# Optimization experiments

Hardware: AMD Instinct MI355X
Metric: run time of the kernel (lower is better)

## Reference

```python
import jax, jax.numpy as jnp
import numpy as np

B, C_IN, C_MID, C_OUT, H, W = 16, 128, 128, 128, 128, 128
DN = ('NCHW', 'OIHW', 'NCHW')


def conv1x1(x, w, b):
    y = jax.lax.conv_general_dilated(x, w, (1, 1), 'VALID', dimension_numbers=DN)
    return y + b[None, :, None, None]


def dwconv3(x, w, b):
    # depthwise 3x3, padding=1, groups = channels
    y = jax.lax.conv_general_dilated(x, w, (1, 1), ((1, 1), (1, 1)),
                                     feature_group_count=x.shape[1],
                                     dimension_numbers=DN)
    return y + b[None, :, None, None]


def setup_inputs() -> dict:
    key = jax.random.key(0)
    ks = jax.random.split(key, 15)
    s = 0.05
    return {
        'x':   jax.random.normal(ks[0], (B, C_IN, H, W), jnp.float32),
        'qw':  jax.random.normal(ks[1], (C_MID, C_IN, 1, 1), jnp.float32) * s,
        'qb':  jax.random.normal(ks[2], (C_MID,), jnp.float32) * s,
        'qdw': jax.random.normal(ks[3], (C_MID, 1, 3, 3), jnp.float32) * s,
        'qdb': jax.random.normal(ks[4], (C_MID,), jnp.float32) * s,
        'kw':  jax.random.normal(ks[5], (C_MID, C_IN, 1, 1), jnp.float32) * s,
        'kb':  jax.random.normal(ks[6], (C_MID,), jnp.float32) * s,
        'kdw': jax.random.normal(ks[7], (C_MID, 1, 3, 3), jnp.float32) * s,
        'kdb': jax.random.normal(ks[8], (C_MID,), jnp.float32) * s,
        'vw':  jax.random.normal(ks[9], (C_MID, C_IN, 1, 1), jnp.float32) * s,
        'vb':  jax.random.normal(ks[10], (C_MID,), jnp.float32) * s,
        'vdw': jax.random.normal(ks[11], (C_MID, 1, 3, 3), jnp.float32) * s,
        'vdb': jax.random.normal(ks[12], (C_MID,), jnp.float32) * s,
        'aw':  jax.random.normal(ks[13], (C_OUT, C_MID, 1, 1), jnp.float32) * s,
        'ab':  jax.random.normal(ks[14], (C_OUT,), jnp.float32) * s,
    }


def reference(x, qw, qb, qdw, qdb, kw, kb, kdw, kdb, vw, vb, vdw, vdb, aw, ab):
    b, c, h, w = x.shape
    q = dwconv3(conv1x1(x, qw, qb), qdw, qdb)
    k = dwconv3(conv1x1(x, kw, kb), kdw, kdb)
    v = dwconv3(conv1x1(x, vw, vb), vdw, vdb)
    # b c h w -> b c (h w)
    q = q.reshape(b, -1, h * w)
    k = k.reshape(b, -1, h * w)
    v = v.reshape(b, -1, h * w)
    # L2-normalize over spatial dim (torch F.normalize: x / max(||x||, eps))
    eps = 1e-12
    q = q / jnp.maximum(jnp.linalg.norm(q, axis=-1, keepdims=True), eps)
    k = k / jnp.maximum(jnp.linalg.norm(k, axis=-1, keepdims=True), eps)
    # channel-wise attention: [b, c, c]
    a = jax.nn.softmax(jnp.einsum('bcn,bdn->bcd', q, k), axis=-1)
    out = jnp.einsum('bcd,bdn->bcn', a, v).reshape(b, -1, h, w)
    return conv1x1(out, aw, ab)
```

## Files before the change

kernel.cpp:

```cpp
#include <hip/hip_runtime.h>

typedef unsigned short u16;
typedef unsigned int u32;
typedef __attribute__((ext_vector_type(8))) __bf16 bf16x8;
typedef __attribute__((ext_vector_type(4))) float f32x4;
typedef __attribute__((ext_vector_type(4))) u32 u32x4;
typedef __attribute__((ext_vector_type(2))) u32 u32x2;

#define HW 16384
#define C 128
#define NB 16
#define LSTR 136
#define FSTR 132

__device__ __forceinline__ u16 f2bf(float f) {
    __bf16 h = (__bf16)f;
    union { __bf16 h; u16 u; } c; c.h = h; return c.u;
}
__device__ __forceinline__ float bf2f(u16 u) {
    union { u32 i; float f; } c; c.i = ((u32)u) << 16; return c.f;
}

__device__ __forceinline__ bf16x8 load_wrow(const float* p) {
    f32x4 a = *(const f32x4*)p, b = *(const f32x4*)(p + 4);
    bf16x8 r;
    #pragma unroll
    for (int i = 0; i < 4; ++i) { r[i] = (__bf16)a[i]; r[i + 4] = (__bf16)b[i]; }
    return r;
}
__device__ __forceinline__ bf16x8 load_wrow(const u16* p) {
    return *(const bf16x8*)p;
}

template <typename WT, typename YT>
__device__ __forceinline__ void gemm128(
    const WT* __restrict__ W, const float* __restrict__ X,
    const float* __restrict__ bias, YT* __restrict__ Y,
    int n0, u16* lds)
{
    const int tid  = threadIdx.x;
    const int lane = tid & 63;
    const int wave = tid >> 6;
    const int m_lo = lane & 15;
    const int quad = lane >> 4;

    #pragma unroll
    for (int r = 0; r < 2; ++r) {
        int idx = tid + 256 * r;
        int n4  = idx & 31;
        int kc  = idx >> 5;
        const float* src = X + (size_t)(kc * 8) * HW + n0 + n4 * 4;
        f32x4 v[8];
        #pragma unroll
        for (int j = 0; j < 8; ++j) v[j] = *(const f32x4*)(src + (size_t)j * HW);
        #pragma unroll
        for (int t = 0; t < 4; ++t) {
            union { u16 u[8]; u32x4 q; } e;
            #pragma unroll
            for (int j = 0; j < 8; ++j) e.u[j] = f2bf(v[j][t]);
            int row = n4 * 4 + t;
            int cs  = kc ^ (n4 & 7);
            *(u32x4*)(lds + row * LSTR + cs * 8) = e.q;
        }
    }
    __syncthreads();

    f32x4 acc[2][8];
    #pragma unroll
    for (int mt = 0; mt < 2; ++mt)
        #pragma unroll
        for (int nt = 0; nt < 8; ++nt) {
            f32x4 z = {0.f, 0.f, 0.f, 0.f};
            acc[mt][nt] = z;
        }

    #pragma unroll
    for (int ks = 0; ks < 4; ++ks) {
        const int k0 = ks * 32 + quad * 8;
        bf16x8 af[2];
        #pragma unroll
        for (int mt = 0; mt < 2; ++mt) {
            int m = wave * 32 + mt * 16 + m_lo;
            af[mt] = load_wrow(W + (size_t)m * 128 + k0);
        }
        #pragma unroll
        for (int nt = 0; nt < 8; ++nt) {
            int n  = nt * 16 + m_lo;
            int cs = (ks * 4 + quad) ^ ((n >> 2) & 7);
            bf16x8 bfrag = *(const bf16x8*)(lds + n * LSTR + cs * 8);
            #pragma unroll
            for (int mt = 0; mt < 2; ++mt)
                acc[mt][nt] = __builtin_amdgcn_mfma_f32_16x16x32_bf16(
                    af[mt], bfrag, acc[mt][nt], 0, 0, 0);
        }
    }
    __syncthreads();

    if constexpr (sizeof(YT) == 2) {
        #pragma unroll
        for (int mt = 0; mt < 2; ++mt)
            #pragma unroll
            for (int nt = 0; nt < 8; ++nt)
                #pragma unroll
                for (int r = 0; r < 4; ++r) {
                    int m = wave * 32 + mt * 16 + quad * 4 + r;
                    int n = nt * 16 + m_lo;
                    lds[m * LSTR + n] = f2bf(acc[mt][nt][r] + bias[m]);
                }
        __syncthreads();
        #pragma unroll
        for (int i = 0; i < 8; ++i) {
            int idx = tid + 256 * i;
            int row = idx >> 4;
            int ch  = idx & 15;
            u32x4 v = *(u32x4*)(lds + row * LSTR + ch * 8);
            *(u32x4*)(Y + (size_t)row * HW + n0 + ch * 8) = v;
        }
    } else {
        float* ldsf = (float*)lds;
        #pragma unroll
        for (int ph = 0; ph < 2; ++ph) {
            if ((wave >> 1) == ph) {
                #pragma unroll
                for (int mt = 0; mt < 2; ++mt)
                    #pragma unroll
                    for (int nt = 0; nt < 8; ++nt)
                        #pragma unroll
                        for (int r = 0; r < 4; ++r) {
                            int m = wave * 32 + mt * 16 + quad * 4 + r;
                            int n = nt * 16 + m_lo;
                            ldsf[(m & 63) * FSTR + n] = acc[mt][nt][r] + bias[m];
                        }
            }
            __syncthreads();
            #pragma unroll
            for (int i = 0; i < 8; ++i) {
                int idx = tid + 256 * i;
                int row = idx >> 5;
                int c4  = idx & 31;
                f32x4 vv = *(const f32x4*)(ldsf + row * FSTR + c4 * 4);
                *(f32x4*)(Y + (size_t)(ph * 64 + row) * HW + n0 + c4 * 4) = vv;
            }
            __syncthreads();
        }
    }
}

__global__ __launch_bounds__(256) void k_conv_qk(
    const float* __restrict__ x,
    const float* __restrict__ qw, const float* __restrict__ qbias,
    const float* __restrict__ kw, const float* __restrict__ kbias,
    u16* __restrict__ qpl, u16* __restrict__ kpl)
{
    __shared__ __align__(16) u16 lds[128 * LSTR];
    int b = blockIdx.z, s = blockIdx.y;
    const float* W    = s ? kw : qw;
    const float* bias = s ? kbias : qbias;
    u16* Y = (s ? kpl : qpl) + (size_t)b * C * HW;
    gemm128(W, x + (size_t)b * C * HW, bias, Y, blockIdx.x * 128, lds);
}

__global__ __launch_bounds__(256) void k_conv_v(
    float* __restrict__ x, const float* __restrict__ vw, const float* __restrict__ vbias)
{
    __shared__ __align__(16) u16 lds[128 * LSTR];
    int b = blockIdx.z;
    float* Xb = x + (size_t)b * C * HW;
    gemm128(vw, Xb, vbias, Xb, blockIdx.x * 128, lds);
}

__global__ __launch_bounds__(256) void k_dw_qk(
    u16* __restrict__ qpl, u16* __restrict__ kpl,
    const float* __restrict__ qdw, const float* __restrict__ qdb,
    const float* __restrict__ kdw, const float* __restrict__ kdb,
    float* __restrict__ norm2)
{
    __shared__ __align__(16) u16 pl[HW];
    __shared__ float red[256];
    int pid = blockIdx.x;
    int s = pid >> 11, bc = pid & 2047, c = bc & 127;
    u16* plane = (s ? kpl : qpl) + (size_t)bc * HW;
    const float* dw = (s ? kdw : qdw) + c * 9;
    float bias = (s ? kdb : qdb)[c];
    int tid = threadIdx.x;

    #pragma unroll
    for (int i = 0; i < 8; ++i) {
        int idx = tid + 256 * i;
        *(u32x4*)(pl + idx * 8) = *(const u32x4*)(plane + idx * 8);
    }
    float w[9];
    #pragma unroll
    for (int j = 0; j < 9; ++j) w[j] = dw[j];
    __syncthreads();

    float ssq = 0.f;
    for (int i = 0; i < 16; ++i) {
        int p0 = (tid + 256 * i) * 4;
        int py = p0 >> 7, px0 = p0 & 127;
        float nb[3][6];
        #pragma unroll
        for (int dy = 0; dy < 3; ++dy) {
            int yy = py + dy - 1;
            bool yok = (yy >= 0) && (yy < 128);
            int ya = yok ? yy : 0;
            #pragma unroll
            for (int j = 0; j < 6; ++j) {
                int xx = px0 + j - 1;
                bool ok = yok && (xx >= 0) && (xx < 128);
                int xa = (xx >= 0 && xx < 128) ? xx : 0;
                float vv = bf2f(pl[ya * 128 + xa]);
                nb[dy][j] = ok ? vv : 0.f;
            }
        }
        u16 o[4];
        #pragma unroll
        for (int t = 0; t < 4; ++t) {
            float acc = bias;
            #pragma unroll
            for (int dy = 0; dy < 3; ++dy)
                #pragma unroll
                for (int dx = 0; dx < 3; ++dx)
                    acc += w[dy * 3 + dx] * nb[dy][t + dx];
            ssq += acc * acc;
            o[t] = f2bf(acc);
        }
        u32x2 pr;
        pr.x = (u32)o[0] | ((u32)o[1] << 16);
        pr.y = (u32)o[2] | ((u32)o[3] << 16);
        *(u32x2*)(plane + p0) = pr;
    }
    red[tid] = ssq;
    __syncthreads();
    for (int off = 128; off > 0; off >>= 1) {
        if (tid < off) red[tid] += red[tid + off];
        __syncthreads();
    }
    if (tid == 0) norm2[s * (NB * C) + bc] = red[0];
}

__global__ __launch_bounds__(256) void k_dw_v(
    float* __restrict__ x, const float* __restrict__ vdw, const float* __restrict__ vdb)
{
    __shared__ __align__(16) float pl[HW];
    int bc = blockIdx.x;
    int c = bc & 127;
    float* plane = x + (size_t)bc * HW;
    const float* dw = vdw + c * 9;
    float bias = vdb[c];
    int tid = threadIdx.x;

    #pragma unroll
    for (int i = 0; i < 16; ++i) {
        int idx = tid + 256 * i;
        *(f32x4*)(pl + idx * 4) = *(const f32x4*)(plane + idx * 4);
    }
    float w[9];
    #pragma unroll
    for (int j = 0; j < 9; ++j) w[j] = dw[j];
    __syncthreads();

    for (int i = 0; i < 16; ++i) {
        int p0 = (tid + 256 * i) * 4;
        int py = p0 >> 7, px0 = p0 & 127;
        float nb[3][6];
        #pragma unroll
        for (int dy = 0; dy < 3; ++dy) {
            int yy = py + dy - 1;
            bool yok = (yy >= 0) && (yy < 128);
            int ya = yok ? yy : 0;
            #pragma unroll
            for (int j = 0; j < 6; ++j) {
                int xx = px0 + j - 1;
                bool ok = yok && (xx >= 0) && (xx < 128);
                int xa = (xx >= 0 && xx < 128) ? xx : 0;
                float vv = pl[ya * 128 + xa];
                nb[dy][j] = ok ? vv : 0.f;
            }
        }
        f32x4 o;
        #pragma unroll
        for (int t = 0; t < 4; ++t) {
            float acc = bias;
            #pragma unroll
            for (int dy = 0; dy < 3; ++dy)
                #pragma unroll
                for (int dx = 0; dx < 3; ++dx)
                    acc += w[dy * 3 + dx] * nb[dy][t + dx];
            o[t] = acc;
        }
        *(f32x4*)(plane + p0) = o;
    }
}

__global__ __launch_bounds__(256) void k_gram(
    const u16* __restrict__ q, const u16* __restrict__ k, float* __restrict__ G)
{
    int kz = blockIdx.x, b = blockIdx.y;
    const u16* qb = q + (size_t)b * C * HW;
    const u16* kb = k + (size_t)b * C * HW;
    int lane = threadIdx.x & 63, wave = threadIdx.x >> 6;
    int m_lo = lane & 15, quad = lane >> 4;
    f32x4 acc[2][8];
    #pragma unroll
    for (int mt = 0; mt < 2; ++mt)
        #pragma unroll
        for (int nt = 0; nt < 8; ++nt) {
            f32x4 z = {0.f, 0.f, 0.f, 0.f};
            acc[mt][nt] = z;
        }
    for (int step = 0; step < 32; ++step) {
        int kk = kz * 1024 + step * 32 + quad * 8;
        bf16x8 a0 = *(const bf16x8*)(qb + (size_t)(wave * 32 + m_lo) * HW + kk);
        bf16x8 a1 = *(const bf16x8*)(qb + (size_t)(wave * 32 + 16 + m_lo) * HW + kk);
        #pragma unroll
        for (int nt = 0; nt < 8; ++nt) {
            bf16x8 bf = *(const bf16x8*)(kb + (size_t)(nt * 16 + m_lo) * HW + kk);
            acc[0][nt] = __builtin_amdgcn_mfma_f32_16x16x32_bf16(a0, bf, acc[0][nt], 0, 0, 0);
            acc[1][nt] = __builtin_amdgcn_mfma_f32_16x16x32_bf16(a1, bf, acc[1][nt], 0, 0, 0);
        }
    }
    float* Gb = G + (size_t)b * C * C;
    #pragma unroll
    for (int mt = 0; mt < 2; ++mt)
        #pragma unroll
        for (int nt = 0; nt < 8; ++nt)
            #pragma unroll
            for (int r = 0; r < 4; ++r) {
                int m = wave * 32 + mt * 16 + quad * 4 + r;
                int n = nt * 16 + m_lo;
                atomicAdd(&Gb[m * C + n], acc[mt][nt][r]);
            }
}

__global__ __launch_bounds__(128) void k_softmax(float* __restrict__ G, const float* __restrict__ norm2)
{
    __shared__ float red[128];
    int c = blockIdx.x, b = blockIdx.y, d = threadIdx.x;
    float* row = G + ((size_t)b * C + c) * C;
    float nq = fmaxf(sqrtf(norm2[b * C + c]), 1e-12f);
    float nk = fmaxf(sqrtf(norm2[NB * C + b * C + d]), 1e-12f);
    float sv = row[d] / (nq * nk);
    red[d] = sv; __syncthreads();
    for (int off = 64; off > 0; off >>= 1) {
        if (d < off) red[d] = fmaxf(red[d], red[d + off]);
        __syncthreads();
    }
    float mx = red[0]; __syncthreads();
    float e = __expf(sv - mx);
    red[d] = e; __syncthreads();
    for (int off = 64; off > 0; off >>= 1) {
        if (d < off) red[d] += red[d + off];
        __syncthreads();
    }
    row[d] = e / red[0];
}

__global__ __launch_bounds__(256) void k_mproj(
    const float* __restrict__ G, const float* __restrict__ aw, u16* __restrict__ M)
{
    __shared__ float As[128 * 16];
    int b = blockIdx.y, d0 = blockIdx.x * 16, tid = threadIdx.x;
    const float* A = G + (size_t)b * C * C;
    #pragma unroll
    for (int i = 0; i < 8; ++i) {
        int idx = tid + 256 * i;
        int cc = idx >> 4, dd = idx & 15;
        As[idx] = A[cc * C + d0 + dd];
    }
    __syncthreads();
    #pragma unroll
    for (int i = 0; i < 8; ++i) {
        int idx = tid + 256 * i;
        int oo = idx >> 4, dd = idx & 15;
        float s = 0.f;
        for (int cc = 0; cc < 128; ++cc)
            s += aw[oo * C + cc] * As[cc * 16 + dd];
        M[((size_t)b * C + oo) * C + d0 + dd] = f2bf(s);
    }
}

__global__ __launch_bounds__(256) void k_out(
    const u16* __restrict__ M, const float* __restrict__ xv,
    const float* __restrict__ ab, float* __restrict__ out)
{
    __shared__ __align__(16) u16 lds[128 * LSTR];
    int b = blockIdx.z;
    gemm128(M + (size_t)b * C * C, xv + (size_t)b * C * HW, ab,
            out + (size_t)b * C * HW, blockIdx.x * 128, lds);
}

extern "C" void kernel_launch(void* const* d_in, const int* in_sizes, int n_in,
                              void* d_out, int out_size, void* d_ws, size_t ws_size,
                              hipStream_t stream)
{
    float* x         = (float*)d_in[0];
    const float* qw  = (const float*)d_in[1];
    const float* qbi = (const float*)d_in[2];
    const float* qdw = (const float*)d_in[3];
    const float* qdb = (const float*)d_in[4];
    const float* kw  = (const float*)d_in[5];
    const float* kbi = (const float*)d_in[6];
    const float* kdw = (const float*)d_in[7];
    const float* kdb = (const float*)d_in[8];
    const float* vw  = (const float*)d_in[9];
    const float* vbi = (const float*)d_in[10];
    const float* vdw = (const float*)d_in[11];
    const float* vdb = (const float*)d_in[12];
    const float* aw  = (const float*)d_in[13];
    const float* ab  = (const float*)d_in[14];

    u16* qpl = (u16*)d_out;
    u16* kpl = qpl + (size_t)NB * C * HW;

    float* G     = (float*)d_ws;
    float* norm2 = G + (size_t)NB * C * C;
    u16*   M     = (u16*)(norm2 + 2 * NB * C);

    hipMemsetAsync(G, 0, (size_t)NB * C * C * sizeof(float), stream);

    k_conv_qk<<<dim3(HW / 128, 2, NB), 256, 0, stream>>>(x, qw, qbi, kw, kbi, qpl, kpl);
    k_conv_v<<<dim3(HW / 128, 1, NB), 256, 0, stream>>>(x, vw, vbi);
    k_dw_qk<<<dim3(2 * NB * C), 256, 0, stream>>>(qpl, kpl, qdw, qdb, kdw, kdb, norm2);
    k_dw_v<<<dim3(NB * C), 256, 0, stream>>>(x, vdw, vdb);
    k_gram<<<dim3(16, NB), 256, 0, stream>>>(qpl, kpl, G);
    k_softmax<<<dim3(C, NB), 128, 0, stream>>>(G, norm2);
    k_mproj<<<dim3(8, NB), 256, 0, stream>>>(G, aw, M);
    k_out<<<dim3(HW / 128, 1, NB), 256, 0, stream>>>(M, x, ab, (float*)d_out);
}
```

Measured before the change: 603.9 us.

## Fuse QKV 1x1 convs into one kernel and fold V depthwise conv into output GEMM

The Q, K and V pointwise convolutions now share a single staged bf16 tile of x in LDS, so x is read once instead of twice. Results are written straight from registers with strided scalar stores instead of going through LDS. The V depthwise 3x3 conv kernel is removed; k_out recomputes it on the fly from neighbouring rows and feeds the result directly into the projection GEMM, saving a full read-write pass over V. The Gram kernel is also split across two N halves to double its block count. The trade-offs are uncoalesced 2-byte and 4-byte global stores in the fused conv and redundant halo reads of V in k_out.

```diff
diff --git a/kernel.cpp b/kernel.cpp
--- a/kernel.cpp
+++ b/kernel.cpp
@@ -32,24 +32,63 @@
     return *(const bf16x8*)p;
 }
 
-template <typename WT, typename YT>
-__device__ __forceinline__ void gemm128(
-    const WT* __restrict__ W, const float* __restrict__ X,
-    const float* __restrict__ bias, YT* __restrict__ Y,
-    int n0, u16* lds)
-{
+template <typename WT>
+__device__ __forceinline__ void mfma_tile(
+    const WT* __restrict__ W, const u16* lds,
+    f32x4 (&acc)[2][8], int wave, int m_lo, int quad)
+{
+    #pragma unroll
+    for (int mt = 0; mt < 2; ++mt)
+        #pragma unroll
+        for (int nt = 0; nt < 8; ++nt) {
+            f32x4 z = {0.f, 0.f, 0.f, 0.f};
+            acc[mt][nt] = z;
+        }
+    #pragma unroll
+    for (int ks = 0; ks < 4; ++ks) {
+        const int k0 = ks * 32 + quad * 8;
+        bf16x8 af[2];
+        #pragma unroll
+        for (int mt = 0; mt < 2; ++mt) {
+            int m = wave * 32 + mt * 16 + m_lo;
+            af[mt] = load_wrow(W + (size_t)m * 128 + k0);
+        }
+        #pragma unroll
+        for (int nt = 0; nt < 8; ++nt) {
+            int n  = nt * 16 + m_lo;
+            int cs = (ks * 4 + quad) ^ ((n >> 2) & 7);
+            bf16x8 bfrag = *(const bf16x8*)(lds + n * LSTR + cs * 8);
+            #pragma unroll
+            for (int mt = 0; mt < 2; ++mt)
+                acc[mt][nt] = __builtin_amdgcn_mfma_f32_16x16x32_bf16(
+                    af[mt], bfrag, acc[mt][nt], 0, 0, 0);
+        }
+    }
+}
+
+__global__ __launch_bounds__(256) void k_conv_qkv(
+    float* __restrict__ x,
+    const float* __restrict__ qw, const float* __restrict__ qbi,
+    const float* __restrict__ kw, const float* __restrict__ kbi,
+    const float* __restrict__ vw, const float* __restrict__ vbi,
+    u16* __restrict__ qpl, u16* __restrict__ kpl)
+{
+    __shared__ __align__(16) u16 lds[128 * LSTR];
     const int tid  = threadIdx.x;
     const int lane = tid & 63;
     const int wave = tid >> 6;
     const int m_lo = lane & 15;
     const int quad = lane >> 4;
+    const int b  = blockIdx.z;
+    const int n0 = blockIdx.x * 128;
+    float* Xb = x + (size_t)b * C * HW;
 
     #pragma unroll
     for (int r = 0; r < 2; ++r) {
         int idx = tid + 256 * r;
         int n4  = idx & 31;
         int kc  = idx >> 5;
-        const float* src = X + (size_t)(kc * 8) * HW + n0 + n4 * 4;
+        const float* src = Xb + (size_t)(kc * 8) * HW + n0 + n4 * 4;
         f32x4 v[8];
         #pragma unroll
         for (int j = 0; j < 8; ++j) v[j] = *(const f32x4*)(src + (size_t)j * HW);
@@ -66,107 +105,38 @@
     __syncthreads();
 
     f32x4 acc[2][8];
+
+    #pragma unroll 1
+    for (int s = 0; s < 2; ++s) {
+        const float* W    = s ? kw : qw;
+        const float* bias = s ? kbi : qbi;
+        u16* Y = (s ? kpl : qpl) + (size_t)b * C * HW;
+        mfma_tile(W, lds, acc, wave, m_lo, quad);
+        #pragma unroll
+        for (int mt = 0; mt < 2; ++mt)
+            #pragma unroll
+            for (int r = 0; r < 4; ++r) {
+                int m = wave * 32 + mt * 16 + quad * 4 + r;
+                float bm = bias[m];
+                u16* rowp = Y + (size_t)m * HW + n0 + m_lo;
+                #pragma unroll
+                for (int nt = 0; nt < 8; ++nt)
+                    rowp[nt * 16] = f2bf(acc[mt][nt][r] + bm);
+            }
+    }
+
+    mfma_tile(vw, lds, acc, wave, m_lo, quad);
     #pragma unroll
     for (int mt = 0; mt < 2; ++mt)
         #pragma unroll
-        for (int nt = 0; nt < 8; ++nt) {
-            f32x4 z = {0.f, 0.f, 0.f, 0.f};
-            acc[mt][nt] = z;
-        }
-
-    #pragma unroll
-    for (int ks = 0; ks < 4; ++ks) {
-        const int k0 = ks * 32 + quad * 8;
-        bf16x8 af[2];
-        #pragma unroll
-        for (int mt = 0; mt < 2; ++mt) {
-            int m = wave * 32 + mt * 16 + m_lo;
-            af[mt] = load_wrow(W + (size_t)m * 128 + k0);
-        }
-        #pragma unroll
-        for (int nt = 0; nt < 8; ++nt) {
-            int n  = nt * 16 + m_lo;
-            int cs = (ks * 4 + quad) ^ ((n >> 2) & 7);
-            bf16x8 bfrag = *(const bf16x8*)(lds + n * LSTR + cs * 8);
-            #pragma unroll
-            for (int mt = 0; mt < 2; ++mt)
-                acc[mt][nt] = __builtin_amdgcn_mfma_f32_16x16x32_bf16(
-                    af[mt], bfrag, acc[mt][nt], 0, 0, 0);
-        }
-    }
-    __syncthreads();
-
-    if constexpr (sizeof(YT) == 2) {
-        #pragma unroll
-        for (int mt = 0; mt < 2; ++mt)
+        for (int r = 0; r < 4; ++r) {
+            int m = wave * 32 + mt * 16 + quad * 4 + r;
+            float bm = vbi[m];
+            float* rowp = Xb + (size_t)m * HW + n0 + m_lo;
             #pragma unroll
             for (int nt = 0; nt < 8; ++nt)
-                #pragma unroll
-                for (int r = 0; r < 4; ++r) {
-                    int m = wave * 32 + mt * 16 + quad * 4 + r;
-                    int n = nt * 16 + m_lo;
-                    lds[m * LSTR + n] = f2bf(acc[mt][nt][r] + bias[m]);
-                }
-        __syncthreads();
-        #pragma unroll
-        for (int i = 0; i < 8; ++i) {
-            int idx = tid + 256 * i;
-            int row = idx >> 4;
-            int ch  = idx & 15;
-            u32x4 v = *(u32x4*)(lds + row * LSTR + ch * 8);
-            *(u32x4*)(Y + (size_t)row * HW + n0 + ch * 8) = v;
-        }
-    } else {
-        float* ldsf = (float*)lds;
-        #pragma unroll
-        for (int ph = 0; ph < 2; ++ph) {
-            if ((wave >> 1) == ph) {
-                #pragma unroll
-                for (int mt = 0; mt < 2; ++mt)
-                    #pragma unroll
-                    for (int nt = 0; nt < 8; ++nt)
-                        #pragma unroll
-                        for (int r = 0; r < 4; ++r) {
-                            int m = wave * 32 + mt * 16 + quad * 4 + r;
-                            int n = nt * 16 + m_lo;
-                            ldsf[(m & 63) * FSTR + n] = acc[mt][nt][r] + bias[m];
-                        }
-            }
-            __syncthreads();
-            #pragma unroll
-            for (int i = 0; i < 8; ++i) {
-                int idx = tid + 256 * i;
-                int row = idx >> 5;
-                int c4  = idx & 31;
-                f32x4 vv = *(const f32x4*)(ldsf + row * FSTR + c4 * 4);
-                *(f32x4*)(Y + (size_t)(ph * 64 + row) * HW + n0 + c4 * 4) = vv;
-            }
-            __syncthreads();
-        }
-    }
-}
-
-__global__ __launch_bounds__(256) void k_conv_qk(
-    const float* __restrict__ x,
-    const float* __restrict__ qw, const float* __restrict__ qbias,
-    const float* __restrict__ kw, const float* __restrict__ kbias,
-    u16* __restrict__ qpl, u16* __restrict__ kpl)
-{
-    __shared__ __align__(16) u16 lds[128 * LSTR];
-    int b = blockIdx.z, s = blockIdx.y;
-    const float* W    = s ? kw : qw;
-    const float* bias = s ? kbias : qbias;
-    u16* Y = (s ? kpl : qpl) + (size_t)b * C * HW;
-    gemm128(W, x + (size_t)b * C * HW, bias, Y, blockIdx.x * 128, lds);
-}
-
-__global__ __launch_bounds__(256) void k_conv_v(
-    float* __restrict__ x, const float* __restrict__ vw, const float* __restrict__ vbias)
-{
-    __shared__ __align__(16) u16 lds[128 * LSTR];
-    int b = blockIdx.z;
-    float* Xb = x + (size_t)b * C * HW;
-    gemm128(vw, Xb, vbias, Xb, blockIdx.x * 128, lds);
+                rowp[nt * 16] = acc[mt][nt][r] + bm;
+        }
 }
 
 __global__ __launch_bounds__(256) void k_dw_qk(
@@ -239,73 +209,19 @@
     if (tid == 0) norm2[s * (NB * C) + bc] = red[0];
 }
 
-__global__ __launch_bounds__(256) void k_dw_v(
-    float* __restrict__ x, const float* __restrict__ vdw, const float* __restrict__ vdb)
-{
-    __shared__ __align__(16) float pl[HW];
-    int bc = blockIdx.x;
-    int c = bc & 127;
-    float* plane = x + (size_t)bc * HW;
-    const float* dw = vdw + c * 9;
-    float bias = vdb[c];
-    int tid = threadIdx.x;
-
-    #pragma unroll
-    for (int i = 0; i < 16; ++i) {
-        int idx = tid + 256 * i;
-        *(f32x4*)(pl + idx * 4) = *(const f32x4*)(plane + idx * 4);
-    }
-    float w[9];
-    #pragma unroll
-    for (int j = 0; j < 9; ++j) w[j] = dw[j];
-    __syncthreads();
-
-    for (int i = 0; i < 16; ++i) {
-        int p0 = (tid + 256 * i) * 4;
-        int py = p0 >> 7, px0 = p0 & 127;
-        float nb[3][6];
-        #pragma unroll
-        for (int dy = 0; dy < 3; ++dy) {
-            int yy = py + dy - 1;
-            bool yok = (yy >= 0) && (yy < 128);
-            int ya = yok ? yy : 0;
-            #pragma unroll
-            for (int j = 0; j < 6; ++j) {
-                int xx = px0 + j - 1;
-                bool ok = yok && (xx >= 0) && (xx < 128);
-                int xa = (xx >= 0 && xx < 128) ? xx : 0;
-                float vv = pl[ya * 128 + xa];
-                nb[dy][j] = ok ? vv : 0.f;
-            }
-        }
-        f32x4 o;
-        #pragma unroll
-        for (int t = 0; t < 4; ++t) {
-            float acc = bias;
-            #pragma unroll
-            for (int dy = 0; dy < 3; ++dy)
-                #pragma unroll
-                for (int dx = 0; dx < 3; ++dx)
-                    acc += w[dy * 3 + dx] * nb[dy][t + dx];
-            o[t] = acc;
-        }
-        *(f32x4*)(plane + p0) = o;
-    }
-}
-
 __global__ __launch_bounds__(256) void k_gram(
     const u16* __restrict__ q, const u16* __restrict__ k, float* __restrict__ G)
 {
-    int kz = blockIdx.x, b = blockIdx.y;
+    int kz = blockIdx.x, nz = blockIdx.y, b = blockIdx.z;
     const u16* qb = q + (size_t)b * C * HW;
     const u16* kb = k + (size_t)b * C * HW;
     int lane = threadIdx.x & 63, wave = threadIdx.x >> 6;
     int m_lo = lane & 15, quad = lane >> 4;
-    f32x4 acc[2][8];
+    f32x4 acc[2][4];
     #pragma unroll
     for (int mt = 0; mt < 2; ++mt)
         #pragma unroll
-        for (int nt = 0; nt < 8; ++nt) {
+        for (int nt = 0; nt < 4; ++nt) {
             f32x4 z = {0.f, 0.f, 0.f, 0.f};
             acc[mt][nt] = z;
         }
@@ -314,8 +230,8 @@
         bf16x8 a0 = *(const bf16x8*)(qb + (size_t)(wave * 32 + m_lo) * HW + kk);
         bf16x8 a1 = *(const bf16x8*)(qb + (size_t)(wave * 32 + 16 + m_lo) * HW + kk);
         #pragma unroll
-        for (int nt = 0; nt < 8; ++nt) {
-            bf16x8 bf = *(const bf16x8*)(kb + (size_t)(nt * 16 + m_lo) * HW + kk);
+        for (int nt = 0; nt < 4; ++nt) {
+            bf16x8 bf = *(const bf16x8*)(kb + (size_t)(nz * 64 + nt * 16 + m_lo) * HW + kk);
             acc[0][nt] = __builtin_amdgcn_mfma_f32_16x16x32_bf16(a0, bf, acc[0][nt], 0, 0, 0);
             acc[1][nt] = __builtin_amdgcn_mfma_f32_16x16x32_bf16(a1, bf, acc[1][nt], 0, 0, 0);
         }
@@ -324,11 +240,11 @@
     #pragma unroll
     for (int mt = 0; mt < 2; ++mt)
         #pragma unroll
-        for (int nt = 0; nt < 8; ++nt)
+        for (int nt = 0; nt < 4; ++nt)
             #pragma unroll
             for (int r = 0; r < 4; ++r) {
                 int m = wave * 32 + mt * 16 + quad * 4 + r;
-                int n = nt * 16 + m_lo;
+                int n = nz * 64 + nt * 16 + m_lo;
                 atomicAdd(&Gb[m * C + n], acc[mt][nt][r]);
             }
 }
@@ -381,13 +297,103 @@
 }
 
 __global__ __launch_bounds__(256) void k_out(
-    const u16* __restrict__ M, const float* __restrict__ xv,
+    const u16* __restrict__ M, const float* __restrict__ v,
+    const float* __restrict__ vdw, const float* __restrict__ vdb,
     const float* __restrict__ ab, float* __restrict__ out)
 {
     __shared__ __align__(16) u16 lds[128 * LSTR];
-    int b = blockIdx.z;
-    gemm128(M + (size_t)b * C * C, xv + (size_t)b * C * HW, ab,
-            out + (size_t)b * C * HW, blockIdx.x * 128, lds);
+    const int tid  = threadIdx.x;
+    const int lane = tid & 63;
+    const int wave = tid >> 6;
+    const int m_lo = lane & 15;
+    const int quad = lane >> 4;
+    const int b   = blockIdx.z;
+    const int row = blockIdx.x;
+    const int n0  = row * 128;
+    const float* Vb = v + (size_t)b * C * HW;
+
+    int rs[3] = { row > 0 ? row - 1 : 0, row, row < 127 ? row + 1 : 127 };
+    float rmask[3] = { row > 0 ? 1.f : 0.f, 1.f, row < 127 ? 1.f : 0.f };
+
+    #pragma unroll
+    for (int it = 0; it < 2; ++it) {
+        int idx = tid + 256 * it;
+        int n8 = idx & 15;
+        int kq = idx >> 4;
+        int p0 = n8 * 8;
+        float lm  = (n8 > 0)  ? 1.f : 0.f;
+        float rmx = (n8 < 15) ? 1.f : 0.f;
+        int pL = (n8 > 0)  ? p0 - 1 : 0;
+        int pR = (n8 < 15) ? p0 + 8 : 127;
+        float o[4][8];
+        #pragma unroll
+        for (int j = 0; j < 4; ++j) {
+            int ch = kq * 4 + j;
+            const float* pw = vdw + ch * 9;
+            float bias = vdb[ch];
+            #pragma unroll
+            for (int t = 0; t < 8; ++t) o[j][t] = bias;
+            const float* plane = Vb + (size_t)ch * HW;
+            #pragma unroll
+            for (int dy = 0; dy < 3; ++dy) {
+                const float* rp = plane + rs[dy] * 128;
+                float rm = rmask[dy];
+                float win[10];
+                f32x4 m0 = *(const f32x4*)(rp + p0);
+                f32x4 m1 = *(const f32x4*)(rp + p0 + 4);
+                win[0] = rp[pL] * lm * rm;
+                win[9] = rp[pR] * rmx * rm;
+                #pragma unroll
+                for (int q2 = 0; q2 < 4; ++q2) { win[1 + q2] = m0[q2] * rm; win[5 + q2] = m1[q2] * rm; }
+                float w0 = pw[dy * 3 + 0], w1 = pw[dy * 3 + 1], w2 = pw[dy * 3 + 2];
+                #pragma unroll
+                for (int t = 0; t < 8; ++t)
+                    o[j][t] += w0 * win[t] + w1 * win[t + 1] + w2 * win[t + 2];
+            }
+        }
+        #pragma unroll
+        for (int t = 0; t < 8; ++t) {
+            int rw  = p0 + t;
+            int n4t = (rw >> 2) & 31;
+            int cs  = (kq >> 1) ^ (n4t & 7);
+            u32x2 e;
+            e.x = (u32)f2bf(o[0][t]) | ((u32)f2bf(o[1][t]) << 16);
+            e.y = (u32)f2bf(o[2][t]) | ((u32)f2bf(o[3][t]) << 16);
+            *(u32x2*)(lds + rw * LSTR + cs * 8 + (kq & 1) * 4) = e;
+        }
+    }
+    __syncthreads();
+
+    f32x4 acc[2][8];
+    mfma_tile(M + (size_t)b * C * C, lds, acc, wave, m_lo, quad);
+    __syncthreads();
+
+    float* ldsf = (float*)lds;
+    #pragma unroll
+    for (int ph = 0; ph < 2; ++ph) {
+        if ((wave >> 1) == ph) {
+            #pragma unroll
+            for (int mt = 0; mt < 2; ++mt)
+                #pragma unroll
+                for (int nt = 0; nt < 8; ++nt)
+                    #pragma unroll
+                    for (int r = 0; r < 4; ++r) {
+                        int m = wave * 32 + mt * 16 + quad * 4 + r;
+                        int n = nt * 16 + m_lo;
+                        ldsf[(m & 63) * FSTR + n] = acc[mt][nt][r] + ab[m];
+                    }
+        }
+        __syncthreads();
+        #pragma unroll
+        for (int i = 0; i < 8; ++i) {
+            int idx = tid + 256 * i;
+            int rw = idx >> 5;
+            int c4 = idx & 31;
+            f32x4 vv = *(const f32x4*)(ldsf + rw * FSTR + c4 * 4);
+            *(f32x4*)(out + (size_t)b * C * HW + (size_t)(ph * 64 + rw) * HW + n0 + c4 * 4) = vv;
+        }
+        __syncthreads();
+    }
 }
 
 extern "C" void kernel_launch(void* const* d_in, const int* in_sizes, int n_in,
@@ -419,12 +425,10 @@
 
     hipMemsetAsync(G, 0, (size_t)NB * C * C * sizeof(float), stream);
 
-    k_conv_qk<<<dim3(HW / 128, 2, NB), 256, 0, stream>>>(x, qw, qbi, kw, kbi, qpl, kpl);
-    k_conv_v<<<dim3(HW / 128, 1, NB), 256, 0, stream>>>(x, vw, vbi);
+    k_conv_qkv<<<dim3(HW / 128, 1, NB), 256, 0, stream>>>(x, qw, qbi, kw, kbi, vw, vbi, qpl, kpl);
     k_dw_qk<<<dim3(2 * NB * C), 256, 0, stream>>>(qpl, kpl, qdw, qdb, kdw, kdb, norm2);
-    k_dw_v<<<dim3(NB * C), 256, 0, stream>>>(x, vdw, vdb);
-    k_gram<<<dim3(16, NB), 256, 0, stream>>>(qpl, kpl, G);
+    k_gram<<<dim3(16, 2, NB), 256, 0, stream>>>(qpl, kpl, G);
     k_softmax<<<dim3(C, NB), 128, 0, stream>>>(G, norm2);
     k_mproj<<<dim3(8, NB), 256, 0, stream>>>(G, aw, M);
-    k_out<<<dim3(HW / 128, 1, NB), 256, 0, stream>>>(M, x, ab, (float*)d_out);
-}
+    k_out<<<dim3(HW / 128, 1, NB), 256, 0, stream>>>(M, x, vdw, vdb, ab, (float*)d_out);
+}
```

Result: faster. 551.4 us (-8.7%).
